# Optimization experiments

Hardware: AMD Instinct MI355X
Metric: run time of the kernel (lower is better)

Reference implementation:

```python
import jax, jax.numpy as jnp
import numpy as np

B, SD, AD, H, QE, NQ = 16384, 512, 64, 1024, 64, 64


def setup_inputs() -> dict:
    key = jax.random.key(0)
    ks = jax.random.split(key, 12)
    s = 0.02
    p = lambda k, shape: (jax.random.normal(k, shape, jnp.float32) * s)
    return {
        "state": jax.random.normal(ks[0], (B, SD), jnp.float32),
        "action": jax.random.normal(ks[1], (B, AD), jnp.float32),
        # twin critics: leading axis 2 stacks q1 / q2 parameters
        "W_e1": p(ks[2], (2, QE, 1)),      "b_e1": p(ks[3], (2, QE)),
        "W_e2": p(ks[4], (2, QE, QE)),     "b_e2": p(ks[5], (2, QE)),
        "W_f1": p(ks[6], (2, H, SD + AD)), "b_f1": p(ks[7], (2, H)),
        "g1": jnp.ones((2, H), jnp.float32),  "beta1": jnp.zeros((2, H), jnp.float32),
        "W_f2": p(ks[8], (2, H, H)),       "b_f2": p(ks[9], (2, H)),
        "g2": jnp.ones((2, H), jnp.float32),  "beta2": jnp.zeros((2, H), jnp.float32),
        "W_h": p(ks[10], (2, 1, H + QE)),  "b_h": p(ks[11], (2, 1)),
    }


def _layernorm(x, g, b, eps=1e-5):
    mu = x.mean(-1, keepdims=True)
    var = ((x - mu) ** 2).mean(-1, keepdims=True)
    return (x - mu) * jax.lax.rsqrt(var + eps) * g + b


def _qnet(state, action, W_e1, b_e1, W_e2, b_e2, W_f1, b_f1, g1, beta1,
          W_f2, b_f2, g2, beta2, W_h, b_h):
    # feature_net (eval mode: dropout is identity)
    x = jnp.concatenate([state, action], axis=-1)            # [B, SD+AD]
    h = jax.nn.relu(_layernorm(x @ W_f1.T + b_f1, g1, beta1))
    feat = jax.nn.relu(_layernorm(h @ W_f2.T + b_f2, g2, beta2))  # [B, H]
    # tau embedding (batch-independent -> compute once per quantile, not per sample)
    tau = (jnp.linspace(0.0, 1.0, NQ + 1)[:-1] + 1.0 / (2 * NQ))[:, None]  # [NQ,1]
    te = jax.nn.relu(tau @ W_e1.T + b_e1) @ W_e2.T + b_e2    # [NQ, QE]
    # head on concat([feat, te]) == linear split (exact same math as the 64-iter loop)
    q_feat = feat @ W_h[0, :H]                               # [B]
    q_tau = te @ W_h[0, H:]                                  # [NQ]
    return q_feat[:, None] + q_tau[None, :] + b_h[0]         # [B, NQ]


def reference(state, action, W_e1, b_e1, W_e2, b_e2, W_f1, b_f1, g1, beta1,
              W_f2, b_f2, g2, beta2, W_h, b_h):
    qnet = lambda *ps: _qnet(state, action, *ps)
    q = jax.vmap(qnet)(W_e1, b_e1, W_e2, b_e2, W_f1, b_f1, g1, beta1,
                       W_f2, b_f2, g2, beta2, W_h, b_h)      # [2, B, NQ]
    return q[0], q[1]
```

## Files before the change

kernel.cpp:

```cpp
#include <hip/hip_runtime.h>
#include <stdint.h>

#define BATCH 16384
#define SDIM 512
#define ADIM 64
#define XDIM 576
#define HDIM 1024
#define NQD 64
#define QED 64

typedef __attribute__((ext_vector_type(8))) short short8;
typedef __attribute__((ext_vector_type(4))) float f32x4;

static __device__ inline unsigned short f2bf(float f) {
  unsigned int u = __float_as_uint(f);
  unsigned int r = (u + 0x7fffu + ((u >> 16) & 1u)) >> 16;
  return (unsigned short)r;
}
static __device__ inline float bf2f(unsigned short u) {
  return __uint_as_float(((unsigned int)u) << 16);
}

static __device__ inline void gload_lds16(const void* g, void* l) {
  __builtin_amdgcn_global_load_lds(
      (const __attribute__((address_space(1))) uint32_t*)g,
      (__attribute__((address_space(3))) uint32_t*)l, 16, 0, 0);
}

#define FENCE() asm volatile("" ::: "memory")


__global__ __launch_bounds__(256) void cvt_x(const float* __restrict__ st,
                                             const float* __restrict__ ac,
                                             unsigned short* __restrict__ xb) {
  const int total = BATCH * XDIM / 4;
  for (int i = blockIdx.x * blockDim.x + threadIdx.x; i < total;
       i += gridDim.x * blockDim.x) {
    const int e = i * 4;
    const int b = e / XDIM;
    const int j = e - b * XDIM;
    float4 v;
    if (j < SDIM) v = *(const float4*)(st + (size_t)b * SDIM + j);
    else          v = *(const float4*)(ac + (size_t)b * ADIM + (j - SDIM));
    ushort4 o;
    o.x = f2bf(v.x); o.y = f2bf(v.y); o.z = f2bf(v.z); o.w = f2bf(v.w);
    ((ushort4*)xb)[i] = o;
  }
}

__global__ __launch_bounds__(256) void cvt_w(const float* __restrict__ src,
                                             unsigned short* __restrict__ dst, int n4) {
  for (int i = blockIdx.x * blockDim.x + threadIdx.x; i < n4;
       i += gridDim.x * blockDim.x) {
    const float4 v = ((const float4*)src)[i];
    ushort4 o;
    o.x = f2bf(v.x); o.y = f2bf(v.y); o.z = f2bf(v.z); o.w = f2bf(v.w);
    ((ushort4*)dst)[i] = o;
  }
}


__global__ void qtau_kernel(const float* __restrict__ We1, const float* __restrict__ be1,
                            const float* __restrict__ We2, const float* __restrict__ be2,
                            const float* __restrict__ Wh,  const float* __restrict__ bh,
                            float* __restrict__ qtau) {
  const int c = blockIdx.x >> 6;
  const int nq = blockIdx.x & 63;
  const int q = threadIdx.x;
  const float tau = (float)nq / 64.0f + 0.0078125f;
  float acc = be2[c * 64 + q];
  for (int e = 0; e < 64; ++e) {
    const float t1 = fmaxf(tau * We1[c * 64 + e] + be1[c * 64 + e], 0.0f);
    acc += t1 * We2[(c * 64 + q) * 64 + e];
  }
  float v = acc * Wh[c * (HDIM + QED) + HDIM + q];
  #pragma unroll
  for (int off = 32; off; off >>= 1) v += __shfl_xor(v, off);
  if (q == 0) qtau[c * 64 + nq] = v + bh[c];
}


template <int K>
__global__ __launch_bounds__(512, 2) void gemm256(const unsigned short* __restrict__ A,
                                                  const unsigned short* __restrict__ W,
                                                  const float* __restrict__ bias,
                                                  unsigned short* __restrict__ C) {
  constexpr int NT = K / 64;
  __shared__ unsigned short Asm[2][256][64];
  __shared__ unsigned short Bsm[2][256][64];

  const int tid  = threadIdx.x;
  const int lane = tid & 63;
  const int wave = tid >> 6;
  const int wm = wave >> 2;
  const int wn = wave & 3;

  const int L = (int)blockIdx.x;
  const int logical = (L & 7) * 32 + (L >> 3);
  const int mBase = (logical >> 2) * 256;
  const int nBase = (logical & 3) * 256;

  const int c0 = wave * 2;
  const int srow  = lane >> 3;
  const int sslot = (lane & 7) ^ (lane >> 3);

  auto stageA = [&](int buf, int h, int kt) {
    const unsigned short* s =
        A + (size_t)(mBase + h * 128 + c0 * 8 + srow) * K + kt * 64 + sslot * 8;
    gload_lds16(s, &Asm[buf][h * 128 + c0 * 8][0]);
    gload_lds16(s + (size_t)8 * K, &Asm[buf][h * 128 + c0 * 8 + 8][0]);
  };
  auto stageB = [&](int buf, int h, int kt) {
    const unsigned short* s =
        W + (size_t)(nBase + h * 128 + c0 * 8 + srow) * K + kt * 64 + sslot * 8;
    gload_lds16(s, &Bsm[buf][h * 128 + c0 * 8][0]);
    gload_lds16(s + (size_t)8 * K, &Bsm[buf][h * 128 + c0 * 8 + 8][0]);
  };

  auto ldA = [&](short8* d, int buf, int mh) {
    #pragma unroll
    for (int fm = 0; fm < 4; ++fm)
      #pragma unroll
      for (int ks = 0; ks < 2; ++ks) {
        const int r = mh * 128 + wm * 64 + fm * 16 + (lane & 15);
        const int ps = (ks * 4 + (lane >> 4)) ^ (r & 7);
        d[fm * 2 + ks] = *(const short8*)&Asm[buf][r][ps * 8];
      }
  };
  auto ldB = [&](short8* d, int buf, int nhalf) {
    #pragma unroll
    for (int fn = 0; fn < 2; ++fn)
      #pragma unroll
      for (int ks = 0; ks < 2; ++ks) {
        const int r = nhalf * 128 + wn * 32 + fn * 16 + (lane & 15);
        const int ps = (ks * 4 + (lane >> 4)) ^ (r & 7);
        d[fn * 2 + ks] = *(const short8*)&Bsm[buf][r][ps * 8];
      }
  };

  f32x4 acc[4][4][2];
  #pragma unroll
  for (int q = 0; q < 4; ++q)
    #pragma unroll
    for (int fm = 0; fm < 4; ++fm)
      #pragma unroll
      for (int fn = 0; fn < 2; ++fn) {
        f32x4 z = {0.f, 0.f, 0.f, 0.f};
        acc[q][fm][fn] = z;
      }

  auto mfmaQ = [&](f32x4 (&aq)[4][2], short8* a, short8* b) {
    #pragma unroll
    for (int fm = 0; fm < 4; ++fm)
      #pragma unroll
      for (int fn = 0; fn < 2; ++fn)
        #pragma unroll
        for (int ks = 0; ks < 2; ++ks)
          aq[fm][fn] = __builtin_amdgcn_mfma_f32_16x16x32_bf16(
              a[fm * 2 + ks], b[fn * 2 + ks], aq[fm][fn], 0, 0, 0);
  };

  stageA(0, 0, 0); stageA(0, 1, 0); stageB(0, 0, 0); stageB(0, 1, 0);
  if (NT > 1) { stageA(1, 0, 1); stageB(1, 1, 1); }

  short8 a[8], b0[4], b1[4];

  for (int t = 0; t < NT; ++t) {
    const int buf = t & 1;
    FENCE();
    if (t == NT - 1) asm volatile("s_waitcnt vmcnt(0)" ::: "memory");
    else             asm volatile("s_waitcnt vmcnt(4)" ::: "memory");
    __builtin_amdgcn_s_barrier();
    FENCE();

    ldA(a, buf, 0);
    ldB(b0, buf, 0);
    if (t + 1 < NT) stageA(buf ^ 1, 1, t + 1);
    FENCE(); __builtin_amdgcn_s_barrier(); FENCE();
    __builtin_amdgcn_s_setprio(1);
    mfmaQ(acc[0], a, b0);
    __builtin_amdgcn_s_setprio(0);
    FENCE(); __builtin_amdgcn_s_barrier(); FENCE();

    ldB(b1, buf, 1);
    if (t + 1 < NT) stageB(buf ^ 1, 0, t + 1);
    FENCE(); __builtin_amdgcn_s_barrier(); FENCE();
    __builtin_amdgcn_s_setprio(1);
    mfmaQ(acc[1], a, b1);
    __builtin_amdgcn_s_setprio(0);
    FENCE(); __builtin_amdgcn_s_barrier(); FENCE();

    ldA(a, buf, 1);
    if (t + 2 < NT) stageA(buf, 0, t + 2);
    FENCE(); __builtin_amdgcn_s_barrier(); FENCE();
    __builtin_amdgcn_s_setprio(1);
    mfmaQ(acc[2], a, b1);
    __builtin_amdgcn_s_setprio(0);
    FENCE(); __builtin_amdgcn_s_barrier(); FENCE();

    if (t + 2 < NT) stageB(buf, 1, t + 2);
    FENCE(); __builtin_amdgcn_s_barrier(); FENCE();
    __builtin_amdgcn_s_setprio(1);
    mfmaQ(acc[3], a, b0);
    __builtin_amdgcn_s_setprio(0);
    FENCE(); __builtin_amdgcn_s_barrier(); FENCE();
  }

  const int MH[4] = {0, 0, 1, 1};
  const int NH[4] = {0, 1, 1, 0};
  #pragma unroll
  for (int q = 0; q < 4; ++q)
    #pragma unroll
    for (int fm = 0; fm < 4; ++fm)
      #pragma unroll
      for (int fn = 0; fn < 2; ++fn) {
        const int col = nBase + NH[q] * 128 + wn * 32 + fn * 16 + (lane & 15);
        const int row0 = mBase + MH[q] * 128 + wm * 64 + fm * 16 + (lane >> 4) * 4;
        const float bv = bias[col];
        #pragma unroll
        for (int j = 0; j < 4; ++j)
          C[(size_t)(row0 + j) * HDIM + col] = f2bf(acc[q][fm][fn][j] + bv);
      }
}


template <bool HEAD>
__global__ __launch_bounds__(256) void ln_head(const unsigned short* __restrict__ X,
                                               const float* __restrict__ g,
                                               const float* __restrict__ bta,
                                               unsigned short* __restrict__ Y,
                                               const float* __restrict__ Wh,
                                               const float* __restrict__ qt,
                                               float* __restrict__ out) {
  const int b = blockIdx.x;
  const int tid = threadIdx.x;
  const int lane = tid & 63;
  const int wave = tid >> 6;
  __shared__ float rs_[4], rq_[4], rp_[4];

  const ushort4 xv = ((const ushort4*)(X + (size_t)b * HDIM))[tid];
  const float x0 = bf2f(xv.x), x1 = bf2f(xv.y), x2 = bf2f(xv.z), x3 = bf2f(xv.w);
  float s = x0 + x1 + x2 + x3;
  float q = x0 * x0 + x1 * x1 + x2 * x2 + x3 * x3;
  #pragma unroll
  for (int off = 32; off; off >>= 1) {
    s += __shfl_xor(s, off);
    q += __shfl_xor(q, off);
  }
  if (lane == 0) { rs_[wave] = s; rq_[wave] = q; }
  __syncthreads();
  s = rs_[0] + rs_[1] + rs_[2] + rs_[3];
  q = rq_[0] + rq_[1] + rq_[2] + rq_[3];
  const float mu = s * (1.0f / 1024.0f);
  const float var = q * (1.0f / 1024.0f) - mu * mu;
  const float rsig = rsqrtf(var + 1e-5f);

  const float4 gv = ((const float4*)g)[tid];
  const float4 bv = ((const float4*)bta)[tid];
  const float y0 = fmaxf((x0 - mu) * rsig * gv.x + bv.x, 0.0f);
  const float y1 = fmaxf((x1 - mu) * rsig * gv.y + bv.y, 0.0f);
  const float y2 = fmaxf((x2 - mu) * rsig * gv.z + bv.z, 0.0f);
  const float y3 = fmaxf((x3 - mu) * rsig * gv.w + bv.w, 0.0f);

  if constexpr (!HEAD) {
    ushort4 o;
    o.x = f2bf(y0); o.y = f2bf(y1); o.z = f2bf(y2); o.w = f2bf(y3);
    ((ushort4*)(Y + (size_t)b * HDIM))[tid] = o;
  } else {
    const float4 wv = ((const float4*)Wh)[tid];
    float p = y0 * wv.x + y1 * wv.y + y2 * wv.z + y3 * wv.w;
    #pragma unroll
    for (int off = 32; off; off >>= 1) p += __shfl_xor(p, off);
    if (lane == 0) rp_[wave] = p;
    __syncthreads();
    if (tid < 64) {
      const float qf = rp_[0] + rp_[1] + rp_[2] + rp_[3];
      out[(size_t)b * NQD + tid] = qf + qt[tid];
    }
  }
}


extern "C" void kernel_launch(void* const* d_in, const int* in_sizes, int n_in,
                              void* d_out, int out_size, void* d_ws, size_t ws_size,
                              hipStream_t stream) {
  (void)in_sizes; (void)n_in; (void)out_size; (void)ws_size;
  const float* state  = (const float*)d_in[0];
  const float* action = (const float*)d_in[1];
  const float* We1 = (const float*)d_in[2];
  const float* be1 = (const float*)d_in[3];
  const float* We2 = (const float*)d_in[4];
  const float* be2 = (const float*)d_in[5];
  const float* Wf1 = (const float*)d_in[6];
  const float* bW1 = (const float*)d_in[7];
  const float* g1  = (const float*)d_in[8];
  const float* bt1 = (const float*)d_in[9];
  const float* Wf2 = (const float*)d_in[10];
  const float* bW2 = (const float*)d_in[11];
  const float* g2  = (const float*)d_in[12];
  const float* bt2 = (const float*)d_in[13];
  const float* Wh  = (const float*)d_in[14];
  const float* bh  = (const float*)d_in[15];
  float* out = (float*)d_out;

  char* ws = (char*)d_ws;
  unsigned short* xb   = (unsigned short*)(ws);
  unsigned short* w1b  = (unsigned short*)(ws + 18874368);
  unsigned short* w2b  = (unsigned short*)(ws + 21233664);
  float*          qtw  = (float*)(ws + 25427968);
  unsigned short* ha   = (unsigned short*)(ws + 25428480);
  unsigned short* hb   = (unsigned short*)(ws + 58982912);

  cvt_x<<<2048, 256, 0, stream>>>(state, action, xb);
  cvt_w<<<1024, 256, 0, stream>>>(Wf1, w1b, 2 * HDIM * XDIM / 4);
  cvt_w<<<1024, 256, 0, stream>>>(Wf2, w2b, 2 * HDIM * HDIM / 4);
  qtau_kernel<<<128, 64, 0, stream>>>(We1, be1, We2, be2, Wh, bh, qtw);

  for (int c = 0; c < 2; ++c) {
    gemm256<XDIM><<<256, 512, 0, stream>>>(
        xb, w1b + (size_t)c * HDIM * XDIM, bW1 + c * HDIM, ha);
    ln_head<false><<<BATCH, 256, 0, stream>>>(
        ha, g1 + c * HDIM, bt1 + c * HDIM, hb, nullptr, nullptr, nullptr);
    gemm256<HDIM><<<256, 512, 0, stream>>>(
        hb, w2b + (size_t)c * HDIM * HDIM, bW2 + c * HDIM, ha);
    ln_head<true><<<BATCH, 256, 0, stream>>>(
        ha, g2 + c * HDIM, bt2 + c * HDIM, nullptr,
        Wh + (size_t)c * (HDIM + QED), qtw + c * 64, out + (size_t)c * BATCH * NQD);
  }
}
```

Baseline: 207.0 us.

## Restructure GEMM main loop with double register buffers and fewer barriers

Reworks the pipelined bf16 MFMA GEMM main loop. It separates A fragments into two register sets and alternates B0 register buffers between even and odd tiles, which lets the last two MFMA quadrants run back to back. This removes several block-wide barriers per K-tile and merges the top-of-loop wait with the end of the previous tile. The cost is higher register pressure and more delicate ordering between LDS overwrites and reads, which could hurt occupancy or correctness.

```diff
diff --git a/kernel.cpp b/kernel.cpp
--- a/kernel.cpp
+++ b/kernel.cpp
@@ -160,50 +160,49 @@
               a[fm * 2 + ks], b[fn * 2 + ks], aq[fm][fn], 0, 0, 0);
   };
 
+  short8 a0[8], a1[8], b0E[4], b0O[4], b1[4];
+
   stageA(0, 0, 0); stageA(0, 1, 0); stageB(0, 0, 0); stageB(0, 1, 0);
   if (NT > 1) { stageA(1, 0, 1); stageB(1, 1, 1); }
-
-  short8 a[8], b0[4], b1[4];
-
-  for (int t = 0; t < NT; ++t) {
+  FENCE();
+  if (NT > 1) asm volatile("s_waitcnt vmcnt(4)" ::: "memory");
+  else        asm volatile("s_waitcnt vmcnt(0)" ::: "memory");
+  __builtin_amdgcn_s_barrier();
+  FENCE();
+
+  auto tile = [&](int t, short8 (&b0)[4]) {
     const int buf = t & 1;
-    FENCE();
-    if (t == NT - 1) asm volatile("s_waitcnt vmcnt(0)" ::: "memory");
-    else             asm volatile("s_waitcnt vmcnt(4)" ::: "memory");
-    __builtin_amdgcn_s_barrier();
-    FENCE();
-
-    ldA(a, buf, 0);
+    ldA(a0, buf, 0);
     ldB(b0, buf, 0);
     if (t + 1 < NT) stageA(buf ^ 1, 1, t + 1);
     FENCE(); __builtin_amdgcn_s_barrier(); FENCE();
     __builtin_amdgcn_s_setprio(1);
-    mfmaQ(acc[0], a, b0);
+    mfmaQ(acc[0], a0, b0);
     __builtin_amdgcn_s_setprio(0);
-    FENCE(); __builtin_amdgcn_s_barrier(); FENCE();
-
     ldB(b1, buf, 1);
     if (t + 1 < NT) stageB(buf ^ 1, 0, t + 1);
     FENCE(); __builtin_amdgcn_s_barrier(); FENCE();
     __builtin_amdgcn_s_setprio(1);
-    mfmaQ(acc[1], a, b1);
+    mfmaQ(acc[1], a0, b1);
     __builtin_amdgcn_s_setprio(0);
-    FENCE(); __builtin_amdgcn_s_barrier(); FENCE();
-
-    ldA(a, buf, 1);
+    ldA(a1, buf, 1);
     if (t + 2 < NT) stageA(buf, 0, t + 2);
     FENCE(); __builtin_amdgcn_s_barrier(); FENCE();
     __builtin_amdgcn_s_setprio(1);
-    mfmaQ(acc[2], a, b1);
+    mfmaQ(acc[2], a1, b1);
+    mfmaQ(acc[3], a1, b0);
     __builtin_amdgcn_s_setprio(0);
-    FENCE(); __builtin_amdgcn_s_barrier(); FENCE();
-
     if (t + 2 < NT) stageB(buf, 1, t + 2);
-    FENCE(); __builtin_amdgcn_s_barrier(); FENCE();
-    __builtin_amdgcn_s_setprio(1);
-    mfmaQ(acc[3], a, b0);
-    __builtin_amdgcn_s_setprio(0);
-    FENCE(); __builtin_amdgcn_s_barrier(); FENCE();
+    FENCE();
+    if (t >= NT - 2) asm volatile("s_waitcnt vmcnt(0)" ::: "memory");
+    else             asm volatile("s_waitcnt vmcnt(4)" ::: "memory");
+    __builtin_amdgcn_s_barrier();
+    FENCE();
+  };
+
+  for (int t = 0; t < NT; t += 2) {
+    tile(t, b0E);
+    if (t + 1 < NT) tile(t + 1, b0O);
   }
 
   const int MH[4] = {0, 0, 1, 1};
```

After: 211.2 us. +2.1%, slower.
